# Kernel optimization log

Hardware: AMD Instinct MI355X
Metric: run time of the kernel (lower is better)

## Reference

```python
import jax, jax.numpy as jnp
from jax import lax
import numpy as np

IGNORE_INDEX = -100


def setup_inputs() -> dict:
    key = jax.random.key(0)
    k1, k2, k3 = jax.random.split(key, 3)
    N, D, V = 8192, 2048, 32000
    x = jax.random.normal(k1, (N, D), dtype=jnp.float32) * (D ** -0.5)
    proj_weight = jax.random.normal(k2, (V, D), dtype=jnp.float32) * (D ** -0.5)
    target = jax.random.randint(k3, (N,), 0, V, dtype=jnp.int64 if jax.config.jax_enable_x64 else jnp.int32)
    return {"x": x, "proj_weight": proj_weight, "target": target, "num_splits": 4}


def reference(x, proj_weight, target, num_splits):
    # Fused linear-projection + cross-entropy, chunked over the token dim so the
    # full [N, V] logits tensor is never materialized (only [N/num_splits, V]).
    N, D = x.shape
    chunk = N // num_splits  # N chosen divisible by num_splits
    x_c = x.reshape(num_splits, chunk, D)
    t_c = target.reshape(num_splits, chunk)

    def body(carry, inp):
        loss_sum, count = carry
        xi, ti = inp  # [chunk, D], [chunk]
        logits = jnp.einsum('nd,vd->nv', xi, proj_weight)  # [chunk, V]
        lse = jax.nn.logsumexp(logits, axis=-1)            # [chunk]
        valid = ti != IGNORE_INDEX
        safe_t = jnp.where(valid, ti, 0)
        tgt_logit = jnp.take_along_axis(logits, safe_t[:, None], axis=-1)[:, 0]
        loss = jnp.where(valid, lse - tgt_logit, 0.0)
        return (loss_sum + loss.sum(), count + valid.sum()), None

    init = (jnp.float32(0.0), jnp.int32(0))
    (loss_sum, count), _ = lax.scan(body, init, (x_c, t_c))
    return loss_sum / count.astype(jnp.float32)  # mean over non-ignored tokens
```

## Files before the change

### kernel.cpp

```cpp
#include <hip/hip_runtime.h>
#include <hip/hip_bf16.h>


typedef __bf16 bf16_t;
typedef bf16_t bf16x8 __attribute__((ext_vector_type(8)));
typedef float f32x4 __attribute__((ext_vector_type(4)));

constexpr int N_TOK = 8192;
constexpr int DIM   = 2048;
constexpr int VOCAB = 32000;
constexpr int BM = 256, BN = 256, BK = 64;
constexpr int MT  = N_TOK / BM;
constexpr int NVT = VOCAB / BN;
constexpr int NKT = DIM / BK;
constexpr int IGNORE_INDEX = -100;

#define GPTR(p) ((const __attribute__((address_space(1))) void*)(p))
#define LPTR(p) ((__attribute__((address_space(3))) void*)(p))

__device__ __forceinline__ bf16_t f2bf(float f) {
  union { float f; unsigned u; } in; in.f = f;
  unsigned u = in.u;
  unsigned r = u + 0x7fffu + ((u >> 16) & 1u);
  union { unsigned short s; bf16_t b; } out;
  out.s = (unsigned short)(r >> 16);
  return out.b;
}

constexpr int XN8 = N_TOK * DIM / 8;
constexpr int WN8 = VOCAB * DIM / 8;

__global__ __launch_bounds__(256) void cvt_both(const float* __restrict__ x,
                                                const float* __restrict__ w,
                                                bf16_t* __restrict__ xb,
                                                bf16_t* __restrict__ wb) {
  int i = blockIdx.x * 256 + threadIdx.x;
  const float* src; bf16_t* dst; int j;
  if (i < XN8) { src = x; dst = xb; j = i; }
  else { j = i - XN8; if (j >= WN8) return; src = w; dst = wb; }
  const float4* s = (const float4*)src;
  float4 a = s[2 * (size_t)j], b = s[2 * (size_t)j + 1];
  bf16x8 o;
  o[0] = f2bf(a.x); o[1] = f2bf(a.y); o[2] = f2bf(a.z); o[3] = f2bf(a.w);
  o[4] = f2bf(b.x); o[5] = f2bf(b.y); o[6] = f2bf(b.z); o[7] = f2bf(b.w);
  *(bf16x8*)(dst + (size_t)j * 8) = o;
}

__global__ __launch_bounds__(512, 2) void fused_gemm_lse(
    const bf16_t* __restrict__ X, const bf16_t* __restrict__ W,
    const int* __restrict__ target,
    float2* __restrict__ partials, float* __restrict__ tgt_logit) {
  __shared__ __align__(16) char smem[131072];

  const int tid  = threadIdx.x;
  const int lane = tid & 63;
  const int wid  = tid >> 6;
  const int wr   = wid >> 2;
  const int wc   = wid & 3;
  const int l15  = lane & 15;
  const int lg   = lane >> 4;

  int bid  = blockIdx.x;
  int wgid = (bid & 7) * (MT * NVT / 8) + (bid >> 3);
  int mt = wgid & (MT - 1);
  int vt = wgid >> 5;
  const int brow = mt * BM;
  const int bcol = vt * BN;

  const bf16_t* Abase = X + (size_t)brow * DIM;
  const bf16_t* Bbase = W + (size_t)bcol * DIM;

  auto stage = [&](const bf16_t* rowbase, int ktile, int ldsoff) {
#pragma unroll
    for (int i = 0; i < 2; ++i) {
      int c = i * 512 + tid;
      int row = c >> 3, cin = c & 7;
      int sc = cin ^ (row & 7);
      const bf16_t* g = rowbase + (size_t)row * DIM + ktile * BK + sc * 8;
      __builtin_amdgcn_global_load_lds(GPTR(g), LPTR(smem + ldsoff + c * 16), 16, 0, 0);
    }
  };
  auto ldA = [&](int slot, int row, int ks) -> bf16x8 {
    int ch = (ks * 4 + lg) ^ (row & 7);
    return *(const bf16x8*)(smem + slot + row * 128 + ch * 16);
  };
  auto ldB = [&](int slot, int row, int ks) -> bf16x8 {
    int ch = (ks * 4 + lg) ^ (row & 7);
    return *(const bf16x8*)(smem + slot + 32768 + row * 128 + ch * 16);
  };

  f32x4 acc[8][4];
#pragma unroll
  for (int m = 0; m < 8; ++m)
#pragma unroll
    for (int n = 0; n < 4; ++n)
      acc[m][n] = (f32x4){0.f, 0.f, 0.f, 0.f};

  stage(Abase,             0, 0);
  stage(Abase + 128 * DIM, 0, 16384);
  stage(Bbase,             0, 32768);
  stage(Bbase + 128 * DIM, 0, 49152);
  stage(Abase,             1, 65536);
  stage(Abase + 128 * DIM, 1, 65536 + 16384);
  asm volatile("s_waitcnt vmcnt(4)" ::: "memory");
  __builtin_amdgcn_s_barrier();

  for (int t = 0; t < NKT; ++t) {
    const int cur = (t & 1) * 65536;
    const int nxt = 65536 - cur;
    const int ktB = (t + 1) & (NKT - 1);
    const int ktA = (t + 2) & (NKT - 1);

    bf16x8 a0[4][2], a1[4][2], b[4][2];

#pragma unroll
    for (int m = 0; m < 4; ++m)
#pragma unroll
      for (int ks = 0; ks < 2; ++ks)
        a0[m][ks] = ldA(cur, wr * 128 + m * 16 + l15, ks);
#pragma unroll
    for (int n = 0; n < 2; ++n)
#pragma unroll
      for (int ks = 0; ks < 2; ++ks)
        b[n][ks] = ldB(cur, wc * 64 + n * 16 + l15, ks);
    stage(Bbase, ktB, nxt + 32768);
    __builtin_amdgcn_s_barrier();
    __builtin_amdgcn_s_setprio(1);
#pragma unroll
    for (int m = 0; m < 4; ++m)
#pragma unroll
      for (int n = 0; n < 2; ++n)
#pragma unroll
        for (int ks = 0; ks < 2; ++ks)
          acc[m][n] = __builtin_amdgcn_mfma_f32_16x16x32_bf16(a0[m][ks], b[n][ks], acc[m][n], 0, 0, 0);
    __builtin_amdgcn_s_setprio(0);
    __builtin_amdgcn_s_barrier();

#pragma unroll
    for (int m = 0; m < 4; ++m)
#pragma unroll
      for (int ks = 0; ks < 2; ++ks)
        a1[m][ks] = ldA(cur, wr * 128 + 64 + m * 16 + l15, ks);
#pragma unroll
    for (int n = 2; n < 4; ++n)
#pragma unroll
      for (int ks = 0; ks < 2; ++ks)
        b[n][ks] = ldB(cur, wc * 64 + n * 16 + l15, ks);
    stage(Bbase + 128 * DIM, ktB, nxt + 49152);
    __builtin_amdgcn_s_barrier();
    __builtin_amdgcn_s_setprio(1);
#pragma unroll
    for (int m = 0; m < 4; ++m)
#pragma unroll
      for (int n = 2; n < 4; ++n)
#pragma unroll
        for (int ks = 0; ks < 2; ++ks)
          acc[m][n] = __builtin_amdgcn_mfma_f32_16x16x32_bf16(a0[m][ks], b[n][ks], acc[m][n], 0, 0, 0);
    __builtin_amdgcn_s_setprio(0);
    __builtin_amdgcn_s_barrier();

    stage(Abase, ktA, cur);
    __builtin_amdgcn_s_barrier();
    __builtin_amdgcn_s_setprio(1);
#pragma unroll
    for (int m = 0; m < 4; ++m)
#pragma unroll
      for (int n = 2; n < 4; ++n)
#pragma unroll
        for (int ks = 0; ks < 2; ++ks)
          acc[m + 4][n] = __builtin_amdgcn_mfma_f32_16x16x32_bf16(a1[m][ks], b[n][ks], acc[m + 4][n], 0, 0, 0);
    __builtin_amdgcn_s_setprio(0);
    __builtin_amdgcn_s_barrier();

    stage(Abase + 128 * DIM, ktA, cur + 16384);
    __builtin_amdgcn_s_barrier();
    __builtin_amdgcn_s_setprio(1);
#pragma unroll
    for (int m = 0; m < 4; ++m)
#pragma unroll
      for (int n = 0; n < 2; ++n)
#pragma unroll
        for (int ks = 0; ks < 2; ++ks)
          acc[m + 4][n] = __builtin_amdgcn_mfma_f32_16x16x32_bf16(a1[m][ks], b[n][ks], acc[m + 4][n], 0, 0, 0);
    __builtin_amdgcn_s_setprio(0);
    asm volatile("s_waitcnt vmcnt(4)" ::: "memory");
    __builtin_amdgcn_s_barrier();
  }

  __syncthreads();
  float* smax = (float*)smem;
  float* ssum = (float*)(smem + 4096);
#pragma unroll
  for (int m = 0; m < 8; ++m) {
#pragma unroll
    for (int i = 0; i < 4; ++i) {
      int rloc = wr * 128 + m * 16 + lg * 4 + i;
      int grow = brow + rloc;
      int tgt  = target[grow];
      float v0 = acc[m][0][i], v1 = acc[m][1][i], v2 = acc[m][2][i], v3 = acc[m][3][i];
      int colbase = bcol + wc * 64 + l15;
      if (colbase      == tgt) tgt_logit[grow] = v0;
      if (colbase + 16 == tgt) tgt_logit[grow] = v1;
      if (colbase + 32 == tgt) tgt_logit[grow] = v2;
      if (colbase + 48 == tgt) tgt_logit[grow] = v3;
      float rmax = fmaxf(fmaxf(v0, v1), fmaxf(v2, v3));
#pragma unroll
      for (int s = 1; s < 16; s <<= 1) rmax = fmaxf(rmax, __shfl_xor(rmax, s));
      float rsum = __expf(v0 - rmax) + __expf(v1 - rmax) +
                   __expf(v2 - rmax) + __expf(v3 - rmax);
#pragma unroll
      for (int s = 1; s < 16; s <<= 1) rsum += __shfl_xor(rsum, s);
      if (l15 == 0) { smax[rloc * 4 + wc] = rmax; ssum[rloc * 4 + wc] = rsum; }
    }
  }
  __syncthreads();
  if (tid < BM) {
    float M = smax[tid * 4], S = ssum[tid * 4];
#pragma unroll
    for (int c = 1; c < 4; ++c) {
      float m2 = smax[tid * 4 + c], s2 = ssum[tid * 4 + c];
      float Mn = fmaxf(M, m2);
      S = S * __expf(M - Mn) + s2 * __expf(m2 - Mn);
      M = Mn;
    }
    partials[(size_t)(brow + tid) * NVT + vt] = make_float2(M, S);
  }
}

__global__ __launch_bounds__(256) void finalize_rows(
    const float2* __restrict__ partials, const float* __restrict__ tgt_logit,
    const int* __restrict__ target, float2* __restrict__ blocksum) {
  int tid = threadIdx.x, lane = tid & 63, w = tid >> 6;
  int row = blockIdx.x * 4 + w;
  float M = -1e30f, S = 0.f;
  for (int i = lane; i < NVT; i += 64) {
    float2 p = partials[(size_t)row * NVT + i];
    float Mn = fmaxf(M, p.x);
    S = S * __expf(M - Mn) + p.y * __expf(p.x - Mn);
    M = Mn;
  }
#pragma unroll
  for (int s = 1; s < 64; s <<= 1) {
    float Mo = __shfl_xor(M, s), So = __shfl_xor(S, s);
    float Mn = fmaxf(M, Mo);
    S = S * __expf(M - Mn) + So * __expf(Mo - Mn);
    M = Mn;
  }
  __shared__ float ls[4], cs[4];
  if (lane == 0) {
    int t = target[row];
    bool valid = (t != IGNORE_INDEX);
    float lse = M + __logf(S);
    ls[w] = valid ? (lse - tgt_logit[row]) : 0.f;
    cs[w] = valid ? 1.f : 0.f;
  }
  __syncthreads();
  if (tid == 0)
    blocksum[blockIdx.x] = make_float2(ls[0] + ls[1] + ls[2] + ls[3],
                                       cs[0] + cs[1] + cs[2] + cs[3]);
}

__global__ __launch_bounds__(256) void finalize_out(
    const float2* __restrict__ blocksum, float* __restrict__ out) {
  int tid = threadIdx.x;
  float s = 0.f, c = 0.f;
  for (int i = tid; i < N_TOK / 4; i += 256) {
    float2 b = blocksum[i];
    s += b.x; c += b.y;
  }
#pragma unroll
  for (int k = 1; k < 64; k <<= 1) { s += __shfl_xor(s, k); c += __shfl_xor(c, k); }
  __shared__ float ss[4], cc[4];
  int w = tid >> 6;
  if ((tid & 63) == 0) { ss[w] = s; cc[w] = c; }
  __syncthreads();
  if (tid == 0) out[0] = (ss[0] + ss[1] + ss[2] + ss[3]) / (cc[0] + cc[1] + cc[2] + cc[3]);
}

extern "C" void kernel_launch(void* const* d_in, const int* in_sizes, int n_in,
                              void* d_out, int out_size, void* d_ws, size_t ws_size,
                              hipStream_t stream) {
  const float* x = (const float*)d_in[0];
  const float* w = (const float*)d_in[1];
  const int* target = (const int*)d_in[2];
  float* out = (float*)d_out;

  char* ws = (char*)d_ws;
  size_t off = 0;
  bf16_t* Xbf = (bf16_t*)(ws + off); off += (size_t)N_TOK * DIM * 2;
  bf16_t* Wbf = (bf16_t*)(ws + off); off += (size_t)VOCAB * DIM * 2;
  float2* partials = (float2*)(ws + off); off += (size_t)N_TOK * NVT * 8;
  float*  tgtlog   = (float*)(ws + off);  off += (size_t)N_TOK * 4;
  float2* blocksum = (float2*)(ws + off); off += (size_t)(N_TOK / 4) * 8;
  (void)ws_size; (void)in_sizes; (void)n_in; (void)out_size;

  int cvt_blocks = (XN8 + WN8 + 255) / 256;
  cvt_both<<<cvt_blocks, 256, 0, stream>>>(x, w, Xbf, Wbf);
  fused_gemm_lse<<<MT * NVT, 512, 0, stream>>>(Xbf, Wbf, target, partials, tgtlog);
  finalize_rows<<<N_TOK / 4, 256, 0, stream>>>(partials, tgtlog, target, blocksum);
  finalize_out<<<1, 256, 0, stream>>>(blocksum, out);
}
```

Measured before the change: 1.508 ms.

## Reschedule GEMM k-loop into templated ping-pong quadrants and grid-stride conversion

Restructures the main k-loop into a templated two-tile body with compile-time LDS slot offsets. The MFMA quadrants are reordered so the A and B fragment loads are split across phases and register use drops. Explicit lgkmcnt waits are added before each MFMA group and the vmcnt wait is moved earlier. The fp32-to-bf16 conversion kernel becomes a grid-stride loop over a fixed 2048 blocks instead of one thread per 8 elements. The goal is better overlap of LDS reads, global-to-LDS staging and MFMA work, but the changed barrier and wait placement could add stalls or correctness hazards.

```diff
diff --git a/kernel.cpp b/kernel.cpp
--- a/kernel.cpp
+++ b/kernel.cpp
@@ -29,21 +29,108 @@
 
 constexpr int XN8 = N_TOK * DIM / 8;
 constexpr int WN8 = VOCAB * DIM / 8;
+constexpr int CVT_BLOCKS = 2048;
 
 __global__ __launch_bounds__(256) void cvt_both(const float* __restrict__ x,
                                                 const float* __restrict__ w,
                                                 bf16_t* __restrict__ xb,
                                                 bf16_t* __restrict__ wb) {
-  int i = blockIdx.x * 256 + threadIdx.x;
-  const float* src; bf16_t* dst; int j;
-  if (i < XN8) { src = x; dst = xb; j = i; }
-  else { j = i - XN8; if (j >= WN8) return; src = w; dst = wb; }
-  const float4* s = (const float4*)src;
-  float4 a = s[2 * (size_t)j], b = s[2 * (size_t)j + 1];
-  bf16x8 o;
-  o[0] = f2bf(a.x); o[1] = f2bf(a.y); o[2] = f2bf(a.z); o[3] = f2bf(a.w);
-  o[4] = f2bf(b.x); o[5] = f2bf(b.y); o[6] = f2bf(b.z); o[7] = f2bf(b.w);
-  *(bf16x8*)(dst + (size_t)j * 8) = o;
+  for (int i = blockIdx.x * 256 + threadIdx.x; i < XN8 + WN8; i += CVT_BLOCKS * 256) {
+    const float* src; bf16_t* dst; int j;
+    if (i < XN8) { src = x; dst = xb; j = i; }
+    else { src = w; dst = wb; j = i - XN8; }
+    const float4* s = (const float4*)src;
+    float4 a = s[2 * (size_t)j], b = s[2 * (size_t)j + 1];
+    bf16x8 o;
+    o[0] = f2bf(a.x); o[1] = f2bf(a.y); o[2] = f2bf(a.z); o[3] = f2bf(a.w);
+    o[4] = f2bf(b.x); o[5] = f2bf(b.y); o[6] = f2bf(b.z); o[7] = f2bf(b.w);
+    *(bf16x8*)(dst + (size_t)j * 8) = o;
+  }
+}
+
+__device__ __forceinline__ void stage_half(const bf16_t* rowbase, int ktile,
+                                           char* smem, int ldsoff, int tid) {
+#pragma unroll
+  for (int i = 0; i < 2; ++i) {
+    int c = i * 512 + tid;
+    int row = c >> 3, cin = c & 7;
+    int sc = cin ^ (row & 7);
+    const bf16_t* g = rowbase + (size_t)row * DIM + ktile * BK + sc * 8;
+    __builtin_amdgcn_global_load_lds(GPTR(g), LPTR(smem + ldsoff + c * 16), 16, 0, 0);
+  }
+}
+
+template <int SLOT>
+__device__ __forceinline__ bf16x8 ldA(const char* smem, int row, int ks, int lg) {
+  int ch = (ks * 4 + lg) ^ (row & 7);
+  return *(const bf16x8*)(smem + SLOT + row * 128 + ch * 16);
+}
+template <int SLOT>
+__device__ __forceinline__ bf16x8 ldB(const char* smem, int row, int ks, int lg) {
+  int ch = (ks * 4 + lg) ^ (row & 7);
+  return *(const bf16x8*)(smem + SLOT + 32768 + row * 128 + ch * 16);
+}
+
+#define MFMA_Q(AVEC, BVEC, MOFF, NOFF)                                          \
+  __builtin_amdgcn_s_setprio(1);                                                \
+  _Pragma("unroll") for (int ks = 0; ks < 2; ++ks)                              \
+    _Pragma("unroll") for (int m = 0; m < 4; ++m)                               \
+      _Pragma("unroll") for (int n = 0; n < 2; ++n)                             \
+        acc[m + MOFF][n + NOFF] = __builtin_amdgcn_mfma_f32_16x16x32_bf16(      \
+            AVEC[m][ks], BVEC[n][ks], acc[m + MOFF][n + NOFF], 0, 0, 0);        \
+  __builtin_amdgcn_s_setprio(0);
+
+#define PRE_MFMA()                                    \
+  __builtin_amdgcn_s_barrier();                       \
+  asm volatile("s_waitcnt lgkmcnt(0)" ::: "memory");
+
+template <int CUR, int NXT>
+__device__ __forceinline__ void tile_body(
+    int ktB, int ktA, const bf16_t* Abase, const bf16_t* Bbase, char* smem,
+    int tid, int wr, int wc, int l15, int lg,
+    bf16x8 (&alo)[4][2], bf16x8 (&ahi)[4][2],
+    bf16x8 (&b01)[2][2], bf16x8 (&b23)[2][2], f32x4 (&acc)[8][4]) {
+#pragma unroll
+  for (int m = 0; m < 4; ++m)
+#pragma unroll
+    for (int ks = 0; ks < 2; ++ks)
+      alo[m][ks] = ldA<CUR>(smem, wr * 128 + m * 16 + l15, ks, lg);
+#pragma unroll
+  for (int n = 0; n < 2; ++n)
+#pragma unroll
+    for (int ks = 0; ks < 2; ++ks)
+      b01[n][ks] = ldB<CUR>(smem, wc * 64 + n * 16 + l15, ks, lg);
+  stage_half(Bbase, ktB, smem, NXT + 32768, tid);
+  asm volatile("s_waitcnt vmcnt(4)" ::: "memory");
+  PRE_MFMA();
+  MFMA_Q(alo, b01, 0, 0);
+  __builtin_amdgcn_s_barrier();
+
+#pragma unroll
+  for (int m = 0; m < 4; ++m)
+#pragma unroll
+    for (int ks = 0; ks < 2; ++ks)
+      ahi[m][ks] = ldA<CUR>(smem, wr * 128 + 64 + m * 16 + l15, ks, lg);
+  stage_half(Bbase + 128 * DIM, ktB, smem, NXT + 49152, tid);
+  PRE_MFMA();
+  MFMA_Q(ahi, b01, 4, 0);
+  __builtin_amdgcn_s_barrier();
+
+#pragma unroll
+  for (int n = 0; n < 2; ++n)
+#pragma unroll
+    for (int ks = 0; ks < 2; ++ks)
+      b23[n][ks] = ldB<CUR>(smem, wc * 64 + (n + 2) * 16 + l15, ks, lg);
+  stage_half(Abase, ktA, smem, CUR, tid);
+  asm volatile("s_waitcnt vmcnt(4)" ::: "memory");
+  PRE_MFMA();
+  MFMA_Q(ahi, b23, 4, 2);
+  __builtin_amdgcn_s_barrier();
+
+  stage_half(Abase + 128 * DIM, ktA, smem, CUR + 16384, tid);
+  PRE_MFMA();
+  MFMA_Q(alo, b23, 0, 2);
+  __builtin_amdgcn_s_barrier();
 }
 
 __global__ __launch_bounds__(512, 2) void fused_gemm_lse(
@@ -70,121 +157,30 @@
   const bf16_t* Abase = X + (size_t)brow * DIM;
   const bf16_t* Bbase = W + (size_t)bcol * DIM;
 
-  auto stage = [&](const bf16_t* rowbase, int ktile, int ldsoff) {
-#pragma unroll
-    for (int i = 0; i < 2; ++i) {
-      int c = i * 512 + tid;
-      int row = c >> 3, cin = c & 7;
-      int sc = cin ^ (row & 7);
-      const bf16_t* g = rowbase + (size_t)row * DIM + ktile * BK + sc * 8;
-      __builtin_amdgcn_global_load_lds(GPTR(g), LPTR(smem + ldsoff + c * 16), 16, 0, 0);
-    }
-  };
-  auto ldA = [&](int slot, int row, int ks) -> bf16x8 {
-    int ch = (ks * 4 + lg) ^ (row & 7);
-    return *(const bf16x8*)(smem + slot + row * 128 + ch * 16);
-  };
-  auto ldB = [&](int slot, int row, int ks) -> bf16x8 {
-    int ch = (ks * 4 + lg) ^ (row & 7);
-    return *(const bf16x8*)(smem + slot + 32768 + row * 128 + ch * 16);
-  };
-
   f32x4 acc[8][4];
 #pragma unroll
   for (int m = 0; m < 8; ++m)
 #pragma unroll
     for (int n = 0; n < 4; ++n)
       acc[m][n] = (f32x4){0.f, 0.f, 0.f, 0.f};
-
-  stage(Abase,             0, 0);
-  stage(Abase + 128 * DIM, 0, 16384);
-  stage(Bbase,             0, 32768);
-  stage(Bbase + 128 * DIM, 0, 49152);
-  stage(Abase,             1, 65536);
-  stage(Abase + 128 * DIM, 1, 65536 + 16384);
+  bf16x8 alo[4][2], ahi[4][2], b01[2][2], b23[2][2];
+
+  stage_half(Abase,             0, smem, 0,             tid);
+  stage_half(Abase + 128 * DIM, 0, smem, 16384,         tid);
+  stage_half(Bbase,             0, smem, 32768,         tid);
+  stage_half(Bbase + 128 * DIM, 0, smem, 49152,         tid);
+  stage_half(Abase,             1, smem, 65536,         tid);
+  stage_half(Abase + 128 * DIM, 1, smem, 65536 + 16384, tid);
   asm volatile("s_waitcnt vmcnt(4)" ::: "memory");
   __builtin_amdgcn_s_barrier();
 
-  for (int t = 0; t < NKT; ++t) {
-    const int cur = (t & 1) * 65536;
-    const int nxt = 65536 - cur;
-    const int ktB = (t + 1) & (NKT - 1);
-    const int ktA = (t + 2) & (NKT - 1);
-
-    bf16x8 a0[4][2], a1[4][2], b[4][2];
-
-#pragma unroll
-    for (int m = 0; m < 4; ++m)
-#pragma unroll
-      for (int ks = 0; ks < 2; ++ks)
-        a0[m][ks] = ldA(cur, wr * 128 + m * 16 + l15, ks);
-#pragma unroll
-    for (int n = 0; n < 2; ++n)
-#pragma unroll
-      for (int ks = 0; ks < 2; ++ks)
-        b[n][ks] = ldB(cur, wc * 64 + n * 16 + l15, ks);
-    stage(Bbase, ktB, nxt + 32768);
-    __builtin_amdgcn_s_barrier();
-    __builtin_amdgcn_s_setprio(1);
-#pragma unroll
-    for (int m = 0; m < 4; ++m)
-#pragma unroll
-      for (int n = 0; n < 2; ++n)
-#pragma unroll
-        for (int ks = 0; ks < 2; ++ks)
-          acc[m][n] = __builtin_amdgcn_mfma_f32_16x16x32_bf16(a0[m][ks], b[n][ks], acc[m][n], 0, 0, 0);
-    __builtin_amdgcn_s_setprio(0);
-    __builtin_amdgcn_s_barrier();
-
-#pragma unroll
-    for (int m = 0; m < 4; ++m)
-#pragma unroll
-      for (int ks = 0; ks < 2; ++ks)
-        a1[m][ks] = ldA(cur, wr * 128 + 64 + m * 16 + l15, ks);
-#pragma unroll
-    for (int n = 2; n < 4; ++n)
-#pragma unroll
-      for (int ks = 0; ks < 2; ++ks)
-        b[n][ks] = ldB(cur, wc * 64 + n * 16 + l15, ks);
-    stage(Bbase + 128 * DIM, ktB, nxt + 49152);
-    __builtin_amdgcn_s_barrier();
-    __builtin_amdgcn_s_setprio(1);
-#pragma unroll
-    for (int m = 0; m < 4; ++m)
-#pragma unroll
-      for (int n = 2; n < 4; ++n)
-#pragma unroll
-        for (int ks = 0; ks < 2; ++ks)
-          acc[m][n] = __builtin_amdgcn_mfma_f32_16x16x32_bf16(a0[m][ks], b[n][ks], acc[m][n], 0, 0, 0);
-    __builtin_amdgcn_s_setprio(0);
-    __builtin_amdgcn_s_barrier();
-
-    stage(Abase, ktA, cur);
-    __builtin_amdgcn_s_barrier();
-    __builtin_amdgcn_s_setprio(1);
-#pragma unroll
-    for (int m = 0; m < 4; ++m)
-#pragma unroll
-      for (int n = 2; n < 4; ++n)
-#pragma unroll
-        for (int ks = 0; ks < 2; ++ks)
-          acc[m + 4][n] = __builtin_amdgcn_mfma_f32_16x16x32_bf16(a1[m][ks], b[n][ks], acc[m + 4][n], 0, 0, 0);
-    __builtin_amdgcn_s_setprio(0);
-    __builtin_amdgcn_s_barrier();
-
-    stage(Abase + 128 * DIM, ktA, cur + 16384);
-    __builtin_amdgcn_s_barrier();
-    __builtin_amdgcn_s_setprio(1);
-#pragma unroll
-    for (int m = 0; m < 4; ++m)
-#pragma unroll
-      for (int n = 0; n < 2; ++n)
-#pragma unroll
-        for (int ks = 0; ks < 2; ++ks)
-          acc[m + 4][n] = __builtin_amdgcn_mfma_f32_16x16x32_bf16(a1[m][ks], b[n][ks], acc[m + 4][n], 0, 0, 0);
-    __builtin_amdgcn_s_setprio(0);
-    asm volatile("s_waitcnt vmcnt(4)" ::: "memory");
-    __builtin_amdgcn_s_barrier();
+  for (int t = 0; t < NKT; t += 2) {
+    tile_body<0, 65536>((t + 1) & (NKT - 1), (t + 2) & (NKT - 1),
+                        Abase, Bbase, smem, tid, wr, wc, l15, lg,
+                        alo, ahi, b01, b23, acc);
+    tile_body<65536, 0>((t + 2) & (NKT - 1), (t + 3) & (NKT - 1),
+                        Abase, Bbase, smem, tid, wr, wc, l15, lg,
+                        alo, ahi, b01, b23, acc);
   }
 
   __syncthreads();
@@ -294,8 +290,7 @@
   float2* blocksum = (float2*)(ws + off); off += (size_t)(N_TOK / 4) * 8;
   (void)ws_size; (void)in_sizes; (void)n_in; (void)out_size;
 
-  int cvt_blocks = (XN8 + WN8 + 255) / 256;
-  cvt_both<<<cvt_blocks, 256, 0, stream>>>(x, w, Xbf, Wbf);
+  cvt_both<<<CVT_BLOCKS, 256, 0, stream>>>(x, w, Xbf, Wbf);
   fused_gemm_lse<<<MT * NVT, 512, 0, stream>>>(Xbf, Wbf, target, partials, tgtlog);
   finalize_rows<<<N_TOK / 4, 256, 0, stream>>>(partials, tgtlog, target, blocksum);
   finalize_out<<<1, 256, 0, stream>>>(blocksum, out);
```

After: 1.485 ms. No clear change (-1.5%).
